# Optimization experiments

Measured on AMD Instinct MI355X. Metric: run time of the kernel, lower is better.

Reference implementation:

```python
import jax, jax.numpy as jnp
import numpy as np

L = 4        # num_blocks
D = 512      # d_model
H = 8        # num_heads
DFF = 2048   # d_ff
EPS = 1.1920929e-07  # torch RMSNorm default eps = finfo(fp32).eps


def setup_inputs() -> dict:
    key = jax.random.key(0)
    ks = jax.random.split(key, 12)
    B, S = 4, 1024
    s = 0.02
    return {
        "x": jax.random.normal(ks[0], (B, S, D), jnp.float32),
        "col_ids": jax.random.randint(ks[1], (B, S), 0, 32),
        "row_ids": jax.random.randint(ks[2], (B, S), 0, 128),
        "nbr_ids": jax.random.randint(ks[3], (B, S), 0, 64),
        # per-block, per-relation attention weights (nn.Linear: y = x @ W.T)
        "Wq": jax.random.normal(ks[4], (L, 4, D, D), jnp.float32) * s,
        "Wk": jax.random.normal(ks[5], (L, 4, D, D), jnp.float32) * s,
        "Wv": jax.random.normal(ks[6], (L, 4, D, D), jnp.float32) * s,
        "Wo": jax.random.normal(ks[7], (L, 4, D, D), jnp.float32) * s,
        # SwiGLU FFN weights per block
        "W1": jax.random.normal(ks[8], (L, DFF, D), jnp.float32) * s,
        "W3": jax.random.normal(ks[9], (L, DFF, D), jnp.float32) * s,
        "W2": jax.random.normal(ks[10], (L, D, DFF), jnp.float32) * s,
        # RMSNorm scales: 4 attn norms + 1 ffn norm per block + final norm_out
        "g_attn": jnp.ones((L, 4, D), jnp.float32),
        "g_ffn": jnp.ones((L, D), jnp.float32),
        "g_out": jnp.ones((D,), jnp.float32),
    }


def _rms(x, g):
    return x * jax.lax.rsqrt(jnp.mean(x * x, axis=-1, keepdims=True) + EPS) * g


def _attn(x, wq, wk, wv, wo, mask):
    # x: [B,S,D]; mask: [B,S,S] bool (True = attend) or None for full attention
    B, S, _ = x.shape
    hd = D // H
    scale = 1.0 / np.sqrt(hd).astype(np.float32)
    q = (x @ wq.T).reshape(B, S, H, hd).transpose(0, 2, 1, 3)  # bhsd
    k = (x @ wk.T).reshape(B, S, H, hd).transpose(0, 2, 1, 3)
    v = (x @ wv.T).reshape(B, S, H, hd).transpose(0, 2, 1, 3)
    sc = jnp.einsum('bhqd,bhkd->bhqk', q, k) * scale
    if mask is not None:
        sc = jnp.where(mask[:, None, :, :], sc, jnp.float32(-1e30))
    a = jax.nn.softmax(sc, axis=-1)
    o = jnp.einsum('bhqk,bhkd->bhqd', a, v).transpose(0, 2, 1, 3).reshape(B, S, D)
    return o @ wo.T


def reference(x, col_ids, row_ids, nbr_ids, Wq, Wk, Wv, Wo, W1, W3, W2, g_attn, g_ffn, g_out):
    # relation order in RelationalBlock: col, feat, nbr, full
    masks = [ids[:, :, None] == ids[:, None, :] for ids in (col_ids, row_ids, nbr_ids)] + [None]
    for l in range(L):
        for r in range(4):
            x = x + _attn(_rms(x, g_attn[l, r]), Wq[l, r], Wk[l, r], Wv[l, r], Wo[l, r], masks[r])
        h = _rms(x, g_ffn[l])
        x = x + (jax.nn.silu(h @ W1[l].T) * (h @ W3[l].T)) @ W2[l].T
    return _rms(x, g_out)
```

## Files before the change

### kernel.cpp

```cpp
#include <hip/hip_runtime.h>
#include <hip/hip_bf16.h>


typedef __attribute__((ext_vector_type(4))) float f32x4;
typedef __attribute__((ext_vector_type(8))) short s16x8;
typedef __attribute__((ext_vector_type(4))) short s16x4;

#define SEQ 1024
#define DM 512
#define MTOT 4096
#define EPSV 1.1920929e-07f

static __device__ __forceinline__ float b2f(short s) {
  unsigned u = ((unsigned)(unsigned short)s) << 16;
  return __builtin_bit_cast(float, u);
}
static __device__ __forceinline__ short f2b(float f) {
  unsigned u = __builtin_bit_cast(unsigned, f);
  u = (u + 0x7fffu + ((u >> 16) & 1u)) >> 16;
  return (short)(unsigned short)u;
}

#define MFMA_BF16(a, b, c) __builtin_amdgcn_mfma_f32_16x16x32_bf16((a), (b), (c), 0, 0, 0)
#define GLLDS(gp, lp)                                                                        \
  __builtin_amdgcn_global_load_lds((const __attribute__((address_space(1))) unsigned*)(gp),  \
                                   (__attribute__((address_space(3))) unsigned*)(lp), 16, 0, 0)
#define GLLDS4(gp, lp)                                                                       \
  __builtin_amdgcn_global_load_lds((const __attribute__((address_space(1))) unsigned*)(gp),  \
                                   (__attribute__((address_space(3))) unsigned*)(lp), 4, 0, 0)

__global__ void cvt_place(const f32x4* __restrict__ src, s16x4* __restrict__ dst, int n4,
                          int shift, int stride4, int off4, float scale) {
  int i = blockIdx.x * 256 + threadIdx.x;
  if (i >= n4) return;
  f32x4 v = src[i];
  s16x4 o;
  o[0] = f2b(v[0] * scale); o[1] = f2b(v[1] * scale);
  o[2] = f2b(v[2] * scale); o[3] = f2b(v[3] * scale);
  int c = i >> shift, r = i & ((1 << shift) - 1);
  dst[(size_t)c * stride4 + off4 + r] = o;
}

template<bool F32OUT>
__global__ void rmsnorm_kernel(const float* __restrict__ x, const float* __restrict__ g,
                               void* __restrict__ outp) {
  int row = blockIdx.x * 4 + (threadIdx.x >> 6);
  int lane = threadIdx.x & 63;
  const float* xr = x + (size_t)row * DM + lane * 8;
  f32x4 a = *(const f32x4*)xr;
  f32x4 b = *(const f32x4*)(xr + 4);
  float ss = a[0]*a[0]+a[1]*a[1]+a[2]*a[2]+a[3]*a[3]+b[0]*b[0]+b[1]*b[1]+b[2]*b[2]+b[3]*b[3];
#pragma unroll
  for (int m = 1; m < 64; m <<= 1) ss += __shfl_xor(ss, m, 64);
  float sc = rsqrtf(ss * (1.0f / DM) + EPSV);
  const float* gp = g + lane * 8;
  if (F32OUT) {
    float* o = (float*)outp + (size_t)row * DM + lane * 8;
    f32x4 o0, o1;
#pragma unroll
    for (int j = 0; j < 4; j++) { o0[j] = a[j] * sc * gp[j]; o1[j] = b[j] * sc * gp[4 + j]; }
    *(f32x4*)o = o0;
    *(f32x4*)(o + 4) = o1;
  } else {
    s16x8 o;
#pragma unroll
    for (int j = 0; j < 4; j++) { o[j] = f2b(a[j] * sc * gp[j]); o[4 + j] = f2b(b[j] * sc * gp[4 + j]); }
    *(s16x8*)((short*)outp + (size_t)row * DM + lane * 8) = o;
  }
}

__global__ void swiglu_kernel(const short* __restrict__ f, short* __restrict__ fa, int n8) {
  int i = blockIdx.x * 256 + threadIdx.x;
  if (i >= n8) return;
  int row = i >> 8, c8 = i & 255;
  s16x8 va = *(const s16x8*)(f + (size_t)row * 4096 + c8 * 8);
  s16x8 vb = *(const s16x8*)(f + (size_t)row * 4096 + 2048 + c8 * 8);
  s16x8 o;
#pragma unroll
  for (int j = 0; j < 8; j++) {
    float xv = b2f(va[j]);
    float yv = b2f(vb[j]);
    float s = xv / (1.0f + __expf(-xv));
    o[j] = f2b(s * yv);
  }
  *(s16x8*)(fa + (size_t)row * 2048 + c8 * 8) = o;
}

template<int AR, int AC, int FUSE>
__global__ __launch_bounds__(256) void gemm_bt(const short* __restrict__ A, const short* __restrict__ W,
                                               short* __restrict__ outb, float* __restrict__ outf,
                                               short* __restrict__ vtb, int N, int K) {
  constexpr int BM = AR * 32;
  constexpr int BN = AC * 32;
  __shared__ short As[BM * 32];
  __shared__ short Bs[BN * 32];
  const int tid = threadIdx.x;
  const int lane = tid & 63;
  const int w = tid >> 6;
  const int wr = w >> 1, wc = w & 1;
  const int m0 = blockIdx.x * BM, n0 = blockIdx.y * BN;
  f32x4 acc[AR][AC] = {};
  for (int k = 0; k < K; k += 32) {
    __syncthreads();
#pragma unroll
    for (int i = 0; i < BM / 64; i++) {
      int s = i * 256 + tid;
      int row = s >> 2, gl = s & 3, gd = gl ^ ((row >> 1) & 3);
      GLLDS(A + (size_t)(m0 + row) * K + k + gd * 8, (char*)As + (i * 256 + w * 64) * 16);
    }
#pragma unroll
    for (int i = 0; i < BN / 64; i++) {
      int s = i * 256 + tid;
      int row = s >> 2, gl = s & 3, gd = gl ^ ((row >> 1) & 3);
      GLLDS(W + (size_t)(n0 + row) * K + k + gd * 8, (char*)Bs + (i * 256 + w * 64) * 16);
    }
    __syncthreads();
    s16x8 af[AR], bf[AC];
#pragma unroll
    for (int i = 0; i < AR; i++) {
      int row = wr * AR * 16 + i * 16 + (lane & 15);
      int gl = (lane >> 4) ^ ((row >> 1) & 3);
      af[i] = *(const s16x8*)(As + row * 32 + gl * 8);
    }
#pragma unroll
    for (int j = 0; j < AC; j++) {
      int row = wc * AC * 16 + j * 16 + (lane & 15);
      int gl = (lane >> 4) ^ ((row >> 1) & 3);
      bf[j] = *(const s16x8*)(Bs + row * 32 + gl * 8);
    }
#pragma unroll
    for (int i = 0; i < AR; i++)
#pragma unroll
      for (int j = 0; j < AC; j++)
        acc[i][j] = MFMA_BF16(af[i], bf[j], acc[i][j]);
  }
#pragma unroll
  for (int i = 0; i < AR; i++) {
    int rbase = m0 + wr * AR * 16 + i * 16 + (lane >> 4) * 4;
#pragma unroll
    for (int j = 0; j < AC; j++) {
      int col = n0 + wc * AC * 16 + j * 16 + (lane & 15);
      if (FUSE == 2 && col >= 1024) {
        int bbv = rbase >> 10, s = rbase & 1023;
        int c = col - 1024, hhv = c >> 6, d = c & 63;
        s16x4 o4;
#pragma unroll
        for (int r = 0; r < 4; r++) o4[r] = f2b(acc[i][j][r]);
        *(s16x4*)(vtb + (((size_t)(bbv * 8 + hhv) * 64 + d) << 10) + s) = o4;
      } else {
#pragma unroll
        for (int r = 0; r < 4; r++) {
          size_t idx = (size_t)(rbase + r) * N + col;
          if (FUSE == 1) outf[idx] += acc[i][j][r];
          else           outb[idx] = f2b(acc[i][j][r]);
        }
      }
    }
  }
}

__global__ __launch_bounds__(256) void attn_kernel(const short* __restrict__ qkv, const short* __restrict__ vt,
                                                   const int* __restrict__ ids, short* __restrict__ Ob) {
  const int bh = blockIdx.x;
  const int bb = bh >> 3, hh = bh & 7;
  const int q0 = blockIdx.y * 64;
  const int tid = threadIdx.x, lane = tid & 63, w = tid >> 6;
  const int g = lane >> 4, qi = lane & 15;
  __shared__ short Kl[64 * 64];
  __shared__ short Vl[64 * 64];
  __shared__ int Kid[64];
  const short* kbase = qkv + 512 + hh * 64;
  const short* vbase = vt + (size_t)bh * 64 * SEQ;
  s16x8 qf0, qf1;
  {
    int qrow = q0 + w * 16 + qi;
    const short* qp = qkv + (size_t)(bb * SEQ + qrow) * 1536 + hh * 64 + g * 8;
    qf0 = *(const s16x8*)qp;
    qf1 = *(const s16x8*)(qp + 32);
  }
  int qid = 0;
  if (ids) qid = ids[bb * SEQ + q0 + w * 16 + qi];
  float m_ = -1e30f, l_ = 0.f;
  f32x4 oacc[4] = {};

  for (int kt = 0; kt < SEQ; kt += 64) {
    __syncthreads();
#pragma unroll
    for (int i = 0; i < 2; i++) {
      int s = i * 256 + tid;
      int row = s >> 3, gl = s & 7, gd = gl ^ (row & 7);
      GLLDS(kbase + (size_t)(bb * SEQ + kt + row) * 1536 + gd * 8, (char*)Kl + (i * 256 + w * 64) * 16);
    }
#pragma unroll
    for (int i = 0; i < 2; i++) {
      int s = i * 256 + tid;
      int row = s >> 3, gl = s & 7, gd = gl ^ (row & 7);
      GLLDS(vbase + (size_t)row * SEQ + kt + gd * 8, (char*)Vl + (i * 256 + w * 64) * 16);
    }
    if (ids && w == 0) GLLDS4(ids + bb * SEQ + kt + lane, (char*)Kid);
    __syncthreads();
    f32x4 sc[4];
#pragma unroll
    for (int kc = 0; kc < 4; kc++) {
      int krow = kc * 16 + qi;
      s16x8 kf0 = *(const s16x8*)(Kl + krow * 64 + ((g ^ (krow & 7)) * 8));
      s16x8 kf1 = *(const s16x8*)(Kl + krow * 64 + (((4 + g) ^ (krow & 7)) * 8));
      f32x4 s4 = {};
      s4 = MFMA_BF16(kf0, qf0, s4);
      s4 = MFMA_BF16(kf1, qf1, s4);
      sc[kc] = s4;
    }
    float p[4][4];
#pragma unroll
    for (int kc = 0; kc < 4; kc++) {
#pragma unroll
      for (int r = 0; r < 4; r++) p[kc][r] = sc[kc][r];
    }
    if (ids) {
#pragma unroll
      for (int kc = 0; kc < 4; kc++) {
        int4 kid4 = *(const int4*)(Kid + kc * 16 + g * 4);
        if (kid4.x != qid) p[kc][0] = -1e30f;
        if (kid4.y != qid) p[kc][1] = -1e30f;
        if (kid4.z != qid) p[kc][2] = -1e30f;
        if (kid4.w != qid) p[kc][3] = -1e30f;
      }
    }
    float mx = fmaxf(fmaxf(p[0][0], p[0][1]), fmaxf(p[0][2], p[0][3]));
#pragma unroll
    for (int kc = 1; kc < 4; kc++)
      mx = fmaxf(mx, fmaxf(fmaxf(p[kc][0], p[kc][1]), fmaxf(p[kc][2], p[kc][3])));
    mx = fmaxf(mx, __shfl_xor(mx, 16, 64));
    mx = fmaxf(mx, __shfl_xor(mx, 32, 64));
    float nm = fmaxf(m_, mx);
    float c = __expf(m_ - nm);
    m_ = nm;
    float sum = 0.f;
#pragma unroll
    for (int kc = 0; kc < 4; kc++) {
#pragma unroll
      for (int r = 0; r < 4; r++) {
        p[kc][r] = __expf(p[kc][r] - nm);
        sum += p[kc][r];
      }
    }
    sum += __shfl_xor(sum, 16, 64);
    sum += __shfl_xor(sum, 32, 64);
    l_ = l_ * c + sum;
#pragma unroll
    for (int r = 0; r < 4; r++) {
      float cr = __shfl(c, g * 4 + r, 16);
      oacc[0][r] *= cr; oacc[1][r] *= cr; oacc[2][r] *= cr; oacc[3][r] *= cr;
    }
    s16x8 pa, pb;
#pragma unroll
    for (int r = 0; r < 4; r++) {
      pa[r] = f2b(p[0][r]); pa[4 + r] = f2b(p[1][r]);
      pb[r] = f2b(p[2][r]); pb[4 + r] = f2b(p[3][r]);
    }
    int sw;
    const short* vrow;
#pragma unroll
    for (int dt = 0; dt < 4; dt++) {
      int dl = dt * 16 + qi;
      sw = dl & 7;
      vrow = Vl + dl * 64;
      s16x4 va0 = *(const s16x4*)(vrow + (((g >> 1) ^ sw) * 8) + (g & 1) * 4);
      s16x4 va1 = *(const s16x4*)(vrow + ((((g >> 1) + 2) ^ sw) * 8) + (g & 1) * 4);
      s16x4 vb0 = *(const s16x4*)(vrow + ((((g >> 1) + 4) ^ sw) * 8) + (g & 1) * 4);
      s16x4 vb1 = *(const s16x4*)(vrow + ((((g >> 1) + 6) ^ sw) * 8) + (g & 1) * 4);
      s16x8 vf0 = {va0[0], va0[1], va0[2], va0[3], va1[0], va1[1], va1[2], va1[3]};
      s16x8 vf1 = {vb0[0], vb0[1], vb0[2], vb0[3], vb1[0], vb1[1], vb1[2], vb1[3]};
      oacc[dt] = MFMA_BF16(pa, vf0, oacc[dt]);
      oacc[dt] = MFMA_BF16(pb, vf1, oacc[dt]);
    }
  }
  const size_t obase = (size_t)(bb * SEQ) * DM + hh * 64;
#pragma unroll
  for (int r = 0; r < 4; r++) {
    float lr = __shfl(l_, g * 4 + r, 16);
    float inv = 1.0f / lr;
    int q = q0 + w * 16 + g * 4 + r;
#pragma unroll
    for (int dt = 0; dt < 4; dt++)
      Ob[obase + (size_t)q * DM + dt * 16 + qi] = f2b(oacc[dt][r] * inv);
  }
}

extern "C" void kernel_launch(void* const* d_in, const int* in_sizes, int n_in,
                              void* d_out, int out_size, void* d_ws, size_t ws_size,
                              hipStream_t stream) {
  const float* x_in  = (const float*)d_in[0];
  const int* col_ids = (const int*)d_in[1];
  const int* row_ids = (const int*)d_in[2];
  const int* nbr_ids = (const int*)d_in[3];
  const float* g_attn = (const float*)d_in[11];
  const float* g_ffn  = (const float*)d_in[12];
  const float* g_out  = (const float*)d_in[13];

  char* ws = (char*)d_ws;
  float* x   = (float*)(ws);
  short* h   = (short*)(ws + (size_t)(8u  << 20));
  short* qkv = (short*)(ws + (size_t)(12u << 20));
  short* vt  = (short*)(ws + (size_t)(24u << 20));
  short* ob  = (short*)(ws + (size_t)(28u << 20));
  short* f   = (short*)(ws + (size_t)(12u << 20));
  short* fa  = (short*)(ws + (size_t)(44u << 20));
  short* wqkv = (short*)(ws + (size_t)(60u  << 20));
  short* wob  = (short*)(ws + (size_t)(84u  << 20));
  short* w13  = (short*)(ws + (size_t)(92u  << 20));
  short* w2b  = (short*)(ws + (size_t)(108u << 20));

  const int N4 = 1048576;
  cvt_place<<<4096, 256, 0, stream>>>((const f32x4*)d_in[4], (s16x4*)wqkv, N4, 16, 196608, 0, 0.125f);
  cvt_place<<<4096, 256, 0, stream>>>((const f32x4*)d_in[5], (s16x4*)wqkv, N4, 16, 196608, 65536, 1.0f);
  cvt_place<<<4096, 256, 0, stream>>>((const f32x4*)d_in[6], (s16x4*)wqkv, N4, 16, 196608, 131072, 1.0f);
  cvt_place<<<4096, 256, 0, stream>>>((const f32x4*)d_in[7], (s16x4*)wob,  N4, 20, 0, 0, 1.0f);
  cvt_place<<<4096, 256, 0, stream>>>((const f32x4*)d_in[8], (s16x4*)w13,  N4, 18, 524288, 0, 1.0f);
  cvt_place<<<4096, 256, 0, stream>>>((const f32x4*)d_in[9], (s16x4*)w13,  N4, 18, 524288, 262144, 1.0f);
  cvt_place<<<4096, 256, 0, stream>>>((const f32x4*)d_in[10], (s16x4*)w2b, N4, 20, 0, 0, 1.0f);

  hipMemcpyAsync(x, x_in, (size_t)MTOT * DM * 4, hipMemcpyDeviceToDevice, stream);

  const int* idsarr[4] = {col_ids, row_ids, nbr_ids, nullptr};

  for (int l = 0; l < 4; l++) {
    for (int r = 0; r < 4; r++) {
      rmsnorm_kernel<false><<<1024, 256, 0, stream>>>(x, g_attn + (size_t)(l * 4 + r) * DM, (void*)h);
      size_t woff = (size_t)(l * 4 + r) * 1536 * DM;
      gemm_bt<4, 2, 2><<<dim3(32, 24), 256, 0, stream>>>(h, wqkv + woff, qkv, nullptr, vt, 1536, DM);
      attn_kernel<<<dim3(32, 16), 256, 0, stream>>>(qkv, vt, idsarr[r], ob);
      gemm_bt<2, 2, 1><<<dim3(64, 8), 256, 0, stream>>>(ob, wob + (size_t)(l * 4 + r) * DM * DM,
                                                        nullptr, x, nullptr, DM, DM);
    }
    rmsnorm_kernel<false><<<1024, 256, 0, stream>>>(x, g_ffn + (size_t)l * DM, (void*)h);
    gemm_bt<4, 4, 0><<<dim3(32, 32), 256, 0, stream>>>(h, w13 + (size_t)l * 4096 * DM, f, nullptr, nullptr, 4096, DM);
    swiglu_kernel<<<4096, 256, 0, stream>>>(f, fa, MTOT * 2048 / 8);
    gemm_bt<2, 2, 1><<<dim3(64, 8), 256, 0, stream>>>(fa, w2b + (size_t)l * DM * 2048, nullptr, x, nullptr, DM, 2048);
  }
  rmsnorm_kernel<true><<<1024, 256, 0, stream>>>(x, g_out, d_out);
}
```

Before: 1.253 ms.

## Fuse SwiGLU into W13 GEMM, enlarge attention tiles, use exp2 with lazy rescale

W1 and W3 rows are interleaved at weight-conversion time, so the W13 GEMM epilogue computes silu(a)*b through a lane shuffle and writes the gated activation directly. This removes the separate SwiGLU kernel and the round trip of the 4096-wide intermediate. The attention kernel moves to 512 threads with 128-query and 128-key tiles. It folds log2(e) into the Q weights so it can use exp2, and it skips the online-softmax rescale unless the running max grows by more than a threshold. The V-transpose layout is permuted to match the new PV fragment loads, which adds coupling between the QKV GEMM epilogue and the attention kernel.

```diff
diff --git a/kernel.cpp b/kernel.cpp
--- a/kernel.cpp
+++ b/kernel.cpp
@@ -10,6 +10,7 @@
 #define DM 512
 #define MTOT 4096
 #define EPSV 1.1920929e-07f
+#define LOG2E 1.44269504088896f
 
 static __device__ __forceinline__ float b2f(short s) {
   unsigned u = ((unsigned)(unsigned short)s) << 16;
@@ -41,6 +42,18 @@
   dst[(size_t)c * stride4 + off4 + r] = o;
 }
 
+__global__ void cvt_w13(const f32x4* __restrict__ src, s16x4* __restrict__ dst, int n4, int off) {
+  int i = blockIdx.x * 256 + threadIdx.x;
+  if (i >= n4) return;
+  f32x4 v = src[i];
+  s16x4 o;
+  o[0] = f2b(v[0]); o[1] = f2b(v[1]); o[2] = f2b(v[2]); o[3] = f2b(v[3]);
+  int srcrow = i >> 7, r = i & 127;
+  int l = srcrow >> 11, n = srcrow & 2047;
+  int dstrow = l * 4096 + n * 2 + off;
+  dst[(size_t)dstrow * 128 + r] = o;
+}
+
 template<bool F32OUT>
 __global__ void rmsnorm_kernel(const float* __restrict__ x, const float* __restrict__ g,
                                void* __restrict__ outp) {
@@ -67,23 +80,6 @@
     for (int j = 0; j < 4; j++) { o[j] = f2b(a[j] * sc * gp[j]); o[4 + j] = f2b(b[j] * sc * gp[4 + j]); }
     *(s16x8*)((short*)outp + (size_t)row * DM + lane * 8) = o;
   }
-}
-
-__global__ void swiglu_kernel(const short* __restrict__ f, short* __restrict__ fa, int n8) {
-  int i = blockIdx.x * 256 + threadIdx.x;
-  if (i >= n8) return;
-  int row = i >> 8, c8 = i & 255;
-  s16x8 va = *(const s16x8*)(f + (size_t)row * 4096 + c8 * 8);
-  s16x8 vb = *(const s16x8*)(f + (size_t)row * 4096 + 2048 + c8 * 8);
-  s16x8 o;
-#pragma unroll
-  for (int j = 0; j < 8; j++) {
-    float xv = b2f(va[j]);
-    float yv = b2f(vb[j]);
-    float s = xv / (1.0f + __expf(-xv));
-    o[j] = f2b(s * yv);
-  }
-  *(s16x8*)(fa + (size_t)row * 2048 + c8 * 8) = o;
 }
 
 template<int AR, int AC, int FUSE>
@@ -143,10 +139,22 @@
       if (FUSE == 2 && col >= 1024) {
         int bbv = rbase >> 10, s = rbase & 1023;
         int c = col - 1024, hhv = c >> 6, d = c & 63;
+        int o = (s & 63) >> 2;
+        int gg = o & 3, h2 = (o >> 2) & 1, q32 = o >> 3;
+        int pnew = q32 * 8 + gg * 2 + h2;
         s16x4 o4;
 #pragma unroll
         for (int r = 0; r < 4; r++) o4[r] = f2b(acc[i][j][r]);
-        *(s16x4*)(vtb + (((size_t)(bbv * 8 + hhv) * 64 + d) << 10) + s) = o4;
+        *(s16x4*)(vtb + (((size_t)(bbv * 8 + hhv) * 64 + d) << 10) + (s & ~63) + pnew * 4) = o4;
+      } else if (FUSE == 3) {
+#pragma unroll
+        for (int r = 0; r < 4; r++) {
+          float own = acc[i][j][r];
+          float other = __shfl_xor(own, 1, 64);
+          float sv = own / (1.0f + __expf(-own));
+          if (!(lane & 1))
+            outb[(size_t)(rbase + r) * (N >> 1) + (col >> 1)] = f2b(sv * other);
+        }
       } else {
 #pragma unroll
         for (int r = 0; r < 4; r++) {
@@ -159,16 +167,16 @@
   }
 }
 
-__global__ __launch_bounds__(256) void attn_kernel(const short* __restrict__ qkv, const short* __restrict__ vt,
+__global__ __launch_bounds__(512) void attn_kernel(const short* __restrict__ qkv, const short* __restrict__ vt,
                                                    const int* __restrict__ ids, short* __restrict__ Ob) {
   const int bh = blockIdx.x;
   const int bb = bh >> 3, hh = bh & 7;
-  const int q0 = blockIdx.y * 64;
+  const int q0 = blockIdx.y * 128;
   const int tid = threadIdx.x, lane = tid & 63, w = tid >> 6;
   const int g = lane >> 4, qi = lane & 15;
-  __shared__ short Kl[64 * 64];
-  __shared__ short Vl[64 * 64];
-  __shared__ int Kid[64];
+  __shared__ short Kl[128 * 64];
+  __shared__ short Vl[64 * 128];
+  __shared__ int Kid[128];
   const short* kbase = qkv + 512 + hh * 64;
   const short* vbase = vt + (size_t)bh * 64 * SEQ;
   s16x8 qf0, qf1;
@@ -183,25 +191,25 @@
   float m_ = -1e30f, l_ = 0.f;
   f32x4 oacc[4] = {};
 
-  for (int kt = 0; kt < SEQ; kt += 64) {
+  for (int kt = 0; kt < SEQ; kt += 128) {
     __syncthreads();
 #pragma unroll
     for (int i = 0; i < 2; i++) {
-      int s = i * 256 + tid;
+      int s = i * 512 + tid;
       int row = s >> 3, gl = s & 7, gd = gl ^ (row & 7);
-      GLLDS(kbase + (size_t)(bb * SEQ + kt + row) * 1536 + gd * 8, (char*)Kl + (i * 256 + w * 64) * 16);
+      GLLDS(kbase + (size_t)(bb * SEQ + kt + row) * 1536 + gd * 8, (char*)Kl + (i * 512 + w * 64) * 16);
     }
 #pragma unroll
     for (int i = 0; i < 2; i++) {
-      int s = i * 256 + tid;
-      int row = s >> 3, gl = s & 7, gd = gl ^ (row & 7);
-      GLLDS(vbase + (size_t)row * SEQ + kt + gd * 8, (char*)Vl + (i * 256 + w * 64) * 16);
-    }
-    if (ids && w == 0) GLLDS4(ids + bb * SEQ + kt + lane, (char*)Kid);
+      int s = i * 512 + tid;
+      int d = s >> 4, gl = s & 15, gd = gl ^ (d & 7);
+      GLLDS(vbase + (size_t)d * SEQ + kt + gd * 8, (char*)Vl + (i * 512 + w * 64) * 16);
+    }
+    if (ids && w < 2) GLLDS4(ids + bb * SEQ + kt + w * 64 + lane, (char*)Kid + w * 256);
     __syncthreads();
-    f32x4 sc[4];
-#pragma unroll
-    for (int kc = 0; kc < 4; kc++) {
+    f32x4 sc[8];
+#pragma unroll
+    for (int kc = 0; kc < 8; kc++) {
       int krow = kc * 16 + qi;
       s16x8 kf0 = *(const s16x8*)(Kl + krow * 64 + ((g ^ (krow & 7)) * 8));
       s16x8 kf1 = *(const s16x8*)(Kl + krow * 64 + (((4 + g) ^ (krow & 7)) * 8));
@@ -210,15 +218,14 @@
       s4 = MFMA_BF16(kf1, qf1, s4);
       sc[kc] = s4;
     }
-    float p[4][4];
-#pragma unroll
-    for (int kc = 0; kc < 4; kc++) {
+    float p[8][4];
+#pragma unroll
+    for (int kc = 0; kc < 8; kc++)
 #pragma unroll
       for (int r = 0; r < 4; r++) p[kc][r] = sc[kc][r];
-    }
     if (ids) {
 #pragma unroll
-      for (int kc = 0; kc < 4; kc++) {
+      for (int kc = 0; kc < 8; kc++) {
         int4 kid4 = *(const int4*)(Kid + kc * 16 + g * 4);
         if (kid4.x != qid) p[kc][0] = -1e30f;
         if (kid4.y != qid) p[kc][1] = -1e30f;
@@ -228,51 +235,49 @@
     }
     float mx = fmaxf(fmaxf(p[0][0], p[0][1]), fmaxf(p[0][2], p[0][3]));
 #pragma unroll
-    for (int kc = 1; kc < 4; kc++)
+    for (int kc = 1; kc < 8; kc++)
       mx = fmaxf(mx, fmaxf(fmaxf(p[kc][0], p[kc][1]), fmaxf(p[kc][2], p[kc][3])));
     mx = fmaxf(mx, __shfl_xor(mx, 16, 64));
     mx = fmaxf(mx, __shfl_xor(mx, 32, 64));
-    float nm = fmaxf(m_, mx);
-    float c = __expf(m_ - nm);
-    m_ = nm;
+    if (__any(mx > m_ + 8.f)) {
+      float nm = fmaxf(m_, mx);
+      float c = exp2f(m_ - nm);
+      m_ = nm;
+      l_ *= c;
+#pragma unroll
+      for (int r = 0; r < 4; r++) {
+        float cr = __shfl(c, g * 4 + r, 16);
+        oacc[0][r] *= cr; oacc[1][r] *= cr; oacc[2][r] *= cr; oacc[3][r] *= cr;
+      }
+    }
     float sum = 0.f;
 #pragma unroll
-    for (int kc = 0; kc < 4; kc++) {
+    for (int kc = 0; kc < 8; kc++)
 #pragma unroll
       for (int r = 0; r < 4; r++) {
-        p[kc][r] = __expf(p[kc][r] - nm);
+        p[kc][r] = exp2f(p[kc][r] - m_);
         sum += p[kc][r];
       }
-    }
     sum += __shfl_xor(sum, 16, 64);
     sum += __shfl_xor(sum, 32, 64);
-    l_ = l_ * c + sum;
-#pragma unroll
-    for (int r = 0; r < 4; r++) {
-      float cr = __shfl(c, g * 4 + r, 16);
-      oacc[0][r] *= cr; oacc[1][r] *= cr; oacc[2][r] *= cr; oacc[3][r] *= cr;
-    }
-    s16x8 pa, pb;
-#pragma unroll
-    for (int r = 0; r < 4; r++) {
-      pa[r] = f2b(p[0][r]); pa[4 + r] = f2b(p[1][r]);
-      pb[r] = f2b(p[2][r]); pb[4 + r] = f2b(p[3][r]);
-    }
-    int sw;
-    const short* vrow;
-#pragma unroll
-    for (int dt = 0; dt < 4; dt++) {
-      int dl = dt * 16 + qi;
-      sw = dl & 7;
-      vrow = Vl + dl * 64;
-      s16x4 va0 = *(const s16x4*)(vrow + (((g >> 1) ^ sw) * 8) + (g & 1) * 4);
-      s16x4 va1 = *(const s16x4*)(vrow + ((((g >> 1) + 2) ^ sw) * 8) + (g & 1) * 4);
-      s16x4 vb0 = *(const s16x4*)(vrow + ((((g >> 1) + 4) ^ sw) * 8) + (g & 1) * 4);
-      s16x4 vb1 = *(const s16x4*)(vrow + ((((g >> 1) + 6) ^ sw) * 8) + (g & 1) * 4);
-      s16x8 vf0 = {va0[0], va0[1], va0[2], va0[3], va1[0], va1[1], va1[2], va1[3]};
-      s16x8 vf1 = {vb0[0], vb0[1], vb0[2], vb0[3], vb1[0], vb1[1], vb1[2], vb1[3]};
-      oacc[dt] = MFMA_BF16(pa, vf0, oacc[dt]);
-      oacc[dt] = MFMA_BF16(pb, vf1, oacc[dt]);
+    l_ += sum;
+#pragma unroll
+    for (int kk = 0; kk < 2; kk++) {
+      s16x8 pa, pb;
+#pragma unroll
+      for (int r = 0; r < 4; r++) {
+        pa[r] = f2b(p[kk * 4 + 0][r]); pa[4 + r] = f2b(p[kk * 4 + 1][r]);
+        pb[r] = f2b(p[kk * 4 + 2][r]); pb[4 + r] = f2b(p[kk * 4 + 3][r]);
+      }
+#pragma unroll
+      for (int dt = 0; dt < 4; dt++) {
+        int dl = dt * 16 + qi;
+        const short* vr = Vl + dl * 128;
+        s16x8 vf0 = *(const s16x8*)(vr + (kk * 8 + (g ^ (dl & 7))) * 8);
+        s16x8 vf1 = *(const s16x8*)(vr + (kk * 8 + ((4 + g) ^ (dl & 7))) * 8);
+        oacc[dt] = MFMA_BF16(pa, vf0, oacc[dt]);
+        oacc[dt] = MFMA_BF16(pb, vf1, oacc[dt]);
+      }
     }
   }
   const size_t obase = (size_t)(bb * SEQ) * DM + hh * 64;
@@ -304,7 +309,6 @@
   short* qkv = (short*)(ws + (size_t)(12u << 20));
   short* vt  = (short*)(ws + (size_t)(24u << 20));
   short* ob  = (short*)(ws + (size_t)(28u << 20));
-  short* f   = (short*)(ws + (size_t)(12u << 20));
   short* fa  = (short*)(ws + (size_t)(44u << 20));
   short* wqkv = (short*)(ws + (size_t)(60u  << 20));
   short* wob  = (short*)(ws + (size_t)(84u  << 20));
@@ -312,12 +316,12 @@
   short* w2b  = (short*)(ws + (size_t)(108u << 20));
 
   const int N4 = 1048576;
-  cvt_place<<<4096, 256, 0, stream>>>((const f32x4*)d_in[4], (s16x4*)wqkv, N4, 16, 196608, 0, 0.125f);
+  cvt_place<<<4096, 256, 0, stream>>>((const f32x4*)d_in[4], (s16x4*)wqkv, N4, 16, 196608, 0, 0.125f * LOG2E);
   cvt_place<<<4096, 256, 0, stream>>>((const f32x4*)d_in[5], (s16x4*)wqkv, N4, 16, 196608, 65536, 1.0f);
   cvt_place<<<4096, 256, 0, stream>>>((const f32x4*)d_in[6], (s16x4*)wqkv, N4, 16, 196608, 131072, 1.0f);
   cvt_place<<<4096, 256, 0, stream>>>((const f32x4*)d_in[7], (s16x4*)wob,  N4, 20, 0, 0, 1.0f);
-  cvt_place<<<4096, 256, 0, stream>>>((const f32x4*)d_in[8], (s16x4*)w13,  N4, 18, 524288, 0, 1.0f);
-  cvt_place<<<4096, 256, 0, stream>>>((const f32x4*)d_in[9], (s16x4*)w13,  N4, 18, 524288, 262144, 1.0f);
+  cvt_w13<<<4096, 256, 0, stream>>>((const f32x4*)d_in[8], (s16x4*)w13, N4, 0);
+  cvt_w13<<<4096, 256, 0, stream>>>((const f32x4*)d_in[9], (s16x4*)w13, N4, 1);
   cvt_place<<<4096, 256, 0, stream>>>((const f32x4*)d_in[10], (s16x4*)w2b, N4, 20, 0, 0, 1.0f);
 
   hipMemcpyAsync(x, x_in, (size_t)MTOT * DM * 4, hipMemcpyDeviceToDevice, stream);
@@ -329,13 +333,12 @@
       rmsnorm_kernel<false><<<1024, 256, 0, stream>>>(x, g_attn + (size_t)(l * 4 + r) * DM, (void*)h);
       size_t woff = (size_t)(l * 4 + r) * 1536 * DM;
       gemm_bt<4, 2, 2><<<dim3(32, 24), 256, 0, stream>>>(h, wqkv + woff, qkv, nullptr, vt, 1536, DM);
-      attn_kernel<<<dim3(32, 16), 256, 0, stream>>>(qkv, vt, idsarr[r], ob);
+      attn_kernel<<<dim3(32, 8), 512, 0, stream>>>(qkv, vt, idsarr[r], ob);
       gemm_bt<2, 2, 1><<<dim3(64, 8), 256, 0, stream>>>(ob, wob + (size_t)(l * 4 + r) * DM * DM,
                                                         nullptr, x, nullptr, DM, DM);
     }
     rmsnorm_kernel<false><<<1024, 256, 0, stream>>>(x, g_ffn + (size_t)l * DM, (void*)h);
-    gemm_bt<4, 4, 0><<<dim3(32, 32), 256, 0, stream>>>(h, w13 + (size_t)l * 4096 * DM, f, nullptr, nullptr, 4096, DM);
-    swiglu_kernel<<<4096, 256, 0, stream>>>(f, fa, MTOT * 2048 / 8);
+    gemm_bt<4, 4, 3><<<dim3(32, 32), 256, 0, stream>>>(h, w13 + (size_t)l * 4096 * DM, fa, nullptr, nullptr, 4096, DM);
     gemm_bt<2, 2, 1><<<dim3(64, 8), 256, 0, stream>>>(fa, w2b + (size_t)l * DM * 2048, nullptr, x, nullptr, DM, 2048);
   }
   rmsnorm_kernel<true><<<1024, 256, 0, stream>>>(x, g_out, d_out);
```

Result: no change. 1.237 ms (-1.3%).
